# Performance work log

Measured on AMD Instinct MI355X. Metric: run time of the kernel, lower is better.

Reference implementation:

```python
import jax, jax.numpy as jnp
import numpy as np

B, S, D = 8, 2048, 256
EXP = 4
NEG = -1e9
EPS = 1e-5


def layer_norm(x, w, b):
    mu = jnp.mean(x, axis=-1, keepdims=True)
    var = jnp.var(x, axis=-1, keepdims=True)
    return (x - mu) * jax.lax.rsqrt(var + EPS) * w + b


def setup_inputs() -> dict:
    key = jax.random.key(0)
    ks = jax.random.split(key, 8)
    x = jax.random.normal(ks[0], (B, S, D), dtype=jnp.float32)
    r_mat = jax.random.normal(ks[1], (B, S, S), dtype=jnp.float32)
    attn_mask = jax.random.randint(ks[2], (S, S), 0, 2).astype(jnp.float32)
    pad_mask = jax.random.randint(ks[3], (B, 1, S), 0, 2).astype(jnp.float32)
    w1 = jax.random.normal(ks[4], (D, EXP * D), dtype=jnp.float32) / np.sqrt(D)
    b1 = jnp.zeros((EXP * D,), dtype=jnp.float32)
    w2 = jax.random.normal(ks[5], (EXP * D, D), dtype=jnp.float32) / np.sqrt(EXP * D)
    b2 = jnp.zeros((D,), dtype=jnp.float32)
    ln1_w = jnp.ones((D,), dtype=jnp.float32)
    ln1_b = jnp.zeros((D,), dtype=jnp.float32)
    ln2_w = jnp.ones((D,), dtype=jnp.float32)
    ln2_b = jnp.zeros((D,), dtype=jnp.float32)
    return {"x": x, "r_mat": r_mat, "attn_mask": attn_mask, "pad_mask": pad_mask,
            "ln1_w": ln1_w, "ln1_b": ln1_b, "ln2_w": ln2_w, "ln2_b": ln2_b,
            "w1": w1, "b1": b1, "w2": w2, "b2": b2}


def reference(x, r_mat, attn_mask, pad_mask, ln1_w, ln1_b, ln2_w, ln2_b, w1, b1, w2, b2):
    # sublayer 0: pre-LN + InrAwaSA + residual
    h = layer_norm(x, ln1_w, ln1_b)                       # [B,S,D]
    scale = jnp.sqrt(jnp.float32(D))
    scores = jnp.einsum("bqd,bkd->bqk", h, h) / scale      # [B,S,S]
    # mask r_mat by pad_mask [B,1,S] and attn_mask [1,S,S], then softmax
    rm = jnp.where(pad_mask == 0.0, NEG, r_mat)
    rm = jnp.where(attn_mask[None] == 0.0, NEG, rm)
    scores = scores + jax.nn.softmax(rm, axis=-1)
    # NOTE: the torch source calls scores.masked_fill(...) non-in-place and
    # discards the result, so scores are NOT re-masked here (faithful no-op).
    prob = jax.nn.softmax(scores, axis=-1)
    x = x + jnp.einsum("bqk,bkd->bqd", prob, h)
    # sublayer 1: pre-LN + FFN + residual (dropout is identity in eval)
    h2 = layer_norm(x, ln2_w, ln2_b)
    ffn = jax.nn.relu(h2 @ w1 + b1) @ w2 + b2
    return x + ffn
```

## Files before the change

kernel.cpp:

```cpp
#include <hip/hip_runtime.h>
#include <stdint.h>

#define NB 8
#define SS 2048
#define DD 256
#define NEGV -1e9f

typedef __attribute__((ext_vector_type(8))) __bf16 bf16x8;
typedef __attribute__((ext_vector_type(4))) float f32x4;

union U16 { uint4 u; bf16x8 b; unsigned short us[8]; };

__device__ __forceinline__ unsigned short tobf(float v) {
  union { float f; uint32_t u; } c; c.f = v;
  uint32_t r = (c.u + 0x7fffu + ((c.u >> 16) & 1u)) >> 16;
  return (unsigned short)r;
}
__device__ __forceinline__ float frombf(unsigned short v) {
  union { uint32_t u; float f; } c; c.u = ((uint32_t)v) << 16;
  return c.f;
}

__device__ __forceinline__ void glds16(const unsigned short* g, unsigned short* l) {
  __builtin_amdgcn_global_load_lds(
      (const __attribute__((address_space(1))) uint32_t*)g,
      (__attribute__((address_space(3))) uint32_t*)l, 16, 0, 0);
}

__device__ __forceinline__ void stage_tile(const unsigned short* src, int ld,
                                           unsigned short* lbuf, int w, int lane) {
  int rl = lane >> 2;
  int cs = (lane & 3) * 8;
  glds16(src + (size_t)(w * 32 + rl) * ld + cs, lbuf + w * 1024);
  glds16(src + (size_t)(w * 32 + 16 + rl) * ld + cs, lbuf + w * 1024 + 512);
}

template <int NSTEPS>
__device__ __forceinline__ void gemm128_tile(
    const unsigned short* __restrict__ A, int lda,
    const unsigned short* __restrict__ Bt, int ldb,
    unsigned short* lA, unsigned short* lB, f32x4 (&acc)[4][4]) {
  const int w = threadIdx.x >> 6, lane = threadIdx.x & 63;
  const int lr = lane & 15, lg = lane >> 4;
  const int wm = w >> 1, wn = w & 1;
#pragma unroll
  for (int i = 0; i < 4; ++i)
#pragma unroll
    for (int j = 0; j < 4; ++j) acc[i][j] = (f32x4){0.f, 0.f, 0.f, 0.f};
  stage_tile(A, lda, lA, w, lane);
  stage_tile(Bt, ldb, lB, w, lane);
  __syncthreads();
  for (int s = 0; s < NSTEPS; ++s) {
    const unsigned short* cA = lA + (s & 1) * 4096;
    const unsigned short* cB = lB + (s & 1) * 4096;
    if (s + 1 < NSTEPS) {
      stage_tile(A + (s + 1) * 32, lda, lA + ((s + 1) & 1) * 4096, w, lane);
      stage_tile(Bt + (s + 1) * 32, ldb, lB + ((s + 1) & 1) * 4096, w, lane);
    }
    bf16x8 am[4], bn[4];
#pragma unroll
    for (int i = 0; i < 4; ++i) {
      U16 u; u.u = *(const uint4*)(cA + (wm * 64 + i * 16 + lr) * 32 + lg * 8);
      am[i] = u.b;
      U16 v; v.u = *(const uint4*)(cB + (wn * 64 + i * 16 + lr) * 32 + lg * 8);
      bn[i] = v.b;
    }
#pragma unroll
    for (int i = 0; i < 4; ++i)
#pragma unroll
      for (int j = 0; j < 4; ++j)
        acc[i][j] = __builtin_amdgcn_mfma_f32_16x16x32_bf16(am[i], bn[j], acc[i][j], 0, 0, 0);
    __syncthreads();
  }
}

__global__ void ln_kernel(const float* __restrict__ in, const float* __restrict__ w,
                          const float* __restrict__ bparm, unsigned short* __restrict__ outb) {
  int row = blockIdx.x * 4 + (threadIdx.x >> 6);
  int lane = threadIdx.x & 63;
  const float* xr = in + (size_t)row * DD;
  float4 v = *(const float4*)(xr + lane * 4);
  float s = v.x + v.y + v.z + v.w;
  float s2 = v.x * v.x + v.y * v.y + v.z * v.z + v.w * v.w;
#pragma unroll
  for (int m = 1; m < 64; m <<= 1) { s += __shfl_xor(s, m); s2 += __shfl_xor(s2, m); }
  float mu = s * (1.f / DD);
  float var = s2 * (1.f / DD) - mu * mu;
  float rs = rsqrtf(var + 1e-5f);
  float4 wv = *(const float4*)(w + lane * 4);
  float4 bv = *(const float4*)(bparm + lane * 4);
  ushort4 o;
  o.x = tobf((v.x - mu) * rs * wv.x + bv.x);
  o.y = tobf((v.y - mu) * rs * wv.y + bv.y);
  o.z = tobf((v.z - mu) * rs * wv.z + bv.z);
  o.w = tobf((v.w - mu) * rs * wv.w + bv.w);
  *(ushort4*)(outb + (size_t)row * DD + lane * 4) = o;
}

__global__ void transpose_kernel(const unsigned short* __restrict__ in,
                                 unsigned short* __restrict__ out) {
  __shared__ unsigned short tile[64][72];
  int bid = blockIdx.x;
  int b = bid >> 7;
  int rest = bid & 127;
  int st = rest >> 2, dt = rest & 3;
  int s0 = st * 64, d0 = dt * 64;
  int t = threadIdx.x;
  int r = t >> 2, cs = (t & 3) * 16;
  const unsigned short* src = in + ((size_t)b * SS + s0 + r) * DD + d0 + cs;
  *(uint4*)&tile[r][cs] = *(const uint4*)src;
  *(uint4*)&tile[r][cs + 8] = *(const uint4*)(src + 8);
  __syncthreads();
  union { unsigned short us[16]; uint4 u[2]; } tmp;
  int dr = t >> 2, sseg = (t & 3) * 16;
#pragma unroll
  for (int j = 0; j < 16; ++j) tmp.us[j] = tile[sseg + j][dr];
  unsigned short* dst = out + ((size_t)b * DD + d0 + dr) * SS + s0 + sseg;
  *(uint4*)dst = tmp.u[0];
  *(uint4*)(dst + 8) = tmp.u[1];
}

__global__ __launch_bounds__(256) void qk_kernel(
    const unsigned short* __restrict__ hb,
    unsigned short* __restrict__ S) {
  __shared__ unsigned short lA[2 * 4096], lB[2 * 4096];
  int bid = blockIdx.x;
  int b = bid & 7;
  int tile = bid >> 3;
  int mb = tile >> 4, nb = tile & 15;
  const unsigned short* A = hb + (size_t)(b * SS + mb * 128) * DD;
  const unsigned short* Bt = hb + (size_t)(b * SS + nb * 128) * DD;
  f32x4 acc[4][4];
  gemm128_tile<8>(A, DD, Bt, DD, lA, lB, acc);
  int w = threadIdx.x >> 6, lane = threadIdx.x & 63;
  int lr = lane & 15, lg = lane >> 4;
  int wm = w >> 1, wn = w & 1;
  unsigned short* Sb = S + (size_t)b * SS * SS;
#pragma unroll
  for (int i = 0; i < 4; ++i)
#pragma unroll
    for (int j = 0; j < 4; ++j)
#pragma unroll
      for (int r = 0; r < 4; ++r) {
        int m = mb * 128 + wm * 64 + i * 16 + lg * 4 + r;
        int n = nb * 128 + wn * 64 + j * 16 + lr;
        Sb[(size_t)m * SS + n] = tobf(acc[i][j][r] * 0.0625f);
      }
}

__global__ __launch_bounds__(256) void smfuse_kernel(
    const float* __restrict__ r_mat,
    const float* __restrict__ attn,
    const float* __restrict__ pad,
    unsigned short* __restrict__ S) {
  int row = blockIdx.x * 4 + (threadIdx.x >> 6);
  int lane = threadIdx.x & 63;
  int b = row >> 11, q = row & 2047;
  const float* rrow = r_mat + (size_t)row * SS;
  const float* arow = attn + (size_t)q * SS;
  const float* prow = pad + (size_t)b * SS;
  unsigned short* srow = S + (size_t)row * SS;

  float rm[32];
  float mx = -__builtin_inff();
#pragma unroll
  for (int i = 0; i < 8; ++i) {
    int c = i * 256 + lane * 4;
    float4 rv = *(const float4*)(rrow + c);
    float4 av = *(const float4*)(arow + c);
    float4 pv = *(const float4*)(prow + c);
    float v0 = (pv.x == 0.f || av.x == 0.f) ? NEGV : rv.x;
    float v1 = (pv.y == 0.f || av.y == 0.f) ? NEGV : rv.y;
    float v2 = (pv.z == 0.f || av.z == 0.f) ? NEGV : rv.z;
    float v3 = (pv.w == 0.f || av.w == 0.f) ? NEGV : rv.w;
    rm[i * 4 + 0] = v0; rm[i * 4 + 1] = v1; rm[i * 4 + 2] = v2; rm[i * 4 + 3] = v3;
    mx = fmaxf(mx, fmaxf(fmaxf(v0, v1), fmaxf(v2, v3)));
  }
#pragma unroll
  for (int m = 1; m < 64; m <<= 1) mx = fmaxf(mx, __shfl_xor(mx, m));
  float sum = 0.f;
#pragma unroll
  for (int j = 0; j < 32; ++j) { rm[j] = __expf(rm[j] - mx); sum += rm[j]; }
#pragma unroll
  for (int m = 1; m < 64; m <<= 1) sum += __shfl_xor(sum, m);
  float inv = 1.f / sum;

  float sc[32];
  float mx2 = -__builtin_inff();
#pragma unroll
  for (int i = 0; i < 8; ++i) {
    int c = i * 256 + lane * 4;
    ushort4 sv = *(const ushort4*)(srow + c);
    float s0 = frombf(sv.x) + rm[i * 4 + 0] * inv;
    float s1 = frombf(sv.y) + rm[i * 4 + 1] * inv;
    float s2 = frombf(sv.z) + rm[i * 4 + 2] * inv;
    float s3 = frombf(sv.w) + rm[i * 4 + 3] * inv;
    sc[i * 4 + 0] = s0; sc[i * 4 + 1] = s1; sc[i * 4 + 2] = s2; sc[i * 4 + 3] = s3;
    mx2 = fmaxf(mx2, fmaxf(fmaxf(s0, s1), fmaxf(s2, s3)));
  }
#pragma unroll
  for (int m = 1; m < 64; m <<= 1) mx2 = fmaxf(mx2, __shfl_xor(mx2, m));
  float sum2 = 0.f;
#pragma unroll
  for (int j = 0; j < 32; ++j) { sc[j] = __expf(sc[j] - mx2); sum2 += sc[j]; }
#pragma unroll
  for (int m = 1; m < 64; m <<= 1) sum2 += __shfl_xor(sum2, m);
  float inv2 = 1.f / sum2;
#pragma unroll
  for (int i = 0; i < 8; ++i) {
    int c = i * 256 + lane * 4;
    ushort4 o;
    o.x = tobf(sc[i * 4 + 0] * inv2);
    o.y = tobf(sc[i * 4 + 1] * inv2);
    o.z = tobf(sc[i * 4 + 2] * inv2);
    o.w = tobf(sc[i * 4 + 3] * inv2);
    *(ushort4*)(srow + c) = o;
  }
}

__global__ __launch_bounds__(256) void pv_kernel(
    const unsigned short* __restrict__ P,
    const unsigned short* __restrict__ hbT,
    unsigned short* __restrict__ pvp) {
  __shared__ unsigned short lA[2 * 4096], lB[2 * 4096];
  int bid = blockIdx.x;
  int b = bid & 7;
  int rest = bid >> 3;
  int ks = rest & 3;
  int rest2 = rest >> 2;
  int nb = rest2 & 1, mb = rest2 >> 1;
  const unsigned short* A = P + (size_t)(b * SS + mb * 128) * SS + ks * 512;
  const unsigned short* Bt = hbT + (size_t)(b * DD + nb * 128) * SS + ks * 512;
  f32x4 acc[4][4];
  gemm128_tile<16>(A, SS, Bt, SS, lA, lB, acc);
  int w = threadIdx.x >> 6, lane = threadIdx.x & 63;
  int lr = lane & 15, lg = lane >> 4;
  int wm = w >> 1, wn = w & 1;
  unsigned short* O = pvp + ((size_t)(ks << 14) + (b << 11)) * DD;
#pragma unroll
  for (int i = 0; i < 4; ++i)
#pragma unroll
    for (int j = 0; j < 4; ++j)
#pragma unroll
      for (int r = 0; r < 4; ++r) {
        int m = mb * 128 + wm * 64 + i * 16 + lg * 4 + r;
        int n = nb * 128 + wn * 64 + j * 16 + lr;
        O[(size_t)m * DD + n] = tobf(acc[i][j][r]);
      }
}

__global__ __launch_bounds__(256) void pvreduce_kernel(
    const unsigned short* __restrict__ pvp,
    const float* __restrict__ x,
    const float* __restrict__ ln2w,
    const float* __restrict__ ln2b,
    float* __restrict__ out,
    unsigned short* __restrict__ h2b) {
  int r = blockIdx.x * 4 + (threadIdx.x >> 6);
  int lane = threadIdx.x & 63;
  int c = lane * 4;
  float o[4] = {0.f, 0.f, 0.f, 0.f};
#pragma unroll
  for (int ks = 0; ks < 4; ++ks) {
    ushort4 pk = *(const ushort4*)(pvp + ((size_t)(ks << 14) + r) * DD + c);
    o[0] += frombf(pk.x); o[1] += frombf(pk.y);
    o[2] += frombf(pk.z); o[3] += frombf(pk.w);
  }
  float4 xv = *(const float4*)(x + (size_t)r * DD + c);
  float val[4] = {o[0] + xv.x, o[1] + xv.y, o[2] + xv.z, o[3] + xv.w};
  float4 ov = {val[0], val[1], val[2], val[3]};
  *(float4*)(out + (size_t)r * DD + c) = ov;
  float s = val[0] + val[1] + val[2] + val[3];
  float s2 = val[0] * val[0] + val[1] * val[1] + val[2] * val[2] + val[3] * val[3];
#pragma unroll
  for (int m = 1; m < 64; m <<= 1) { s += __shfl_xor(s, m); s2 += __shfl_xor(s2, m); }
  float mu = s * (1.f / DD);
  float var = s2 * (1.f / DD) - mu * mu;
  float rsv = rsqrtf(var + 1e-5f);
  float4 wv = *(const float4*)(ln2w + c);
  float4 bv = *(const float4*)(ln2b + c);
  ushort4 h;
  h.x = tobf((val[0] - mu) * rsv * wv.x + bv.x);
  h.y = tobf((val[1] - mu) * rsv * wv.y + bv.y);
  h.z = tobf((val[2] - mu) * rsv * wv.z + bv.z);
  h.w = tobf((val[3] - mu) * rsv * wv.w + bv.w);
  *(ushort4*)(h2b + (size_t)r * DD + c) = h;
}

__global__ void wconv_kernel(const float* __restrict__ src, unsigned short* __restrict__ dst,
                             int K, int N) {
  int k = blockIdx.x;
  for (int n = threadIdx.x; n < N; n += 256)
    dst[(size_t)n * K + k] = tobf(src[(size_t)k * N + n]);
}

__global__ __launch_bounds__(256) void ffn1_kernel(
    const unsigned short* __restrict__ A0,
    const unsigned short* __restrict__ Bt0,
    const float* __restrict__ bias,
    unsigned short* __restrict__ Out) {
  __shared__ unsigned short lA[2 * 4096], lB[2 * 4096];
  int bid = blockIdx.x;
  int nb = bid & 7, mb = bid >> 3;
  const unsigned short* A = A0 + (size_t)(mb * 128) * 256;
  const unsigned short* Bt = Bt0 + (size_t)(nb * 128) * 256;
  f32x4 acc[4][4];
  gemm128_tile<8>(A, 256, Bt, 256, lA, lB, acc);
  int w = threadIdx.x >> 6, lane = threadIdx.x & 63;
  int lr = lane & 15, lg = lane >> 4;
  int wm = w >> 1, wn = w & 1;
#pragma unroll
  for (int i = 0; i < 4; ++i)
#pragma unroll
    for (int j = 0; j < 4; ++j)
#pragma unroll
      for (int r = 0; r < 4; ++r) {
        int m = mb * 128 + wm * 64 + i * 16 + lg * 4 + r;
        int n = nb * 128 + wn * 64 + j * 16 + lr;
        float v = fmaxf(acc[i][j][r] + bias[n], 0.f);
        Out[(size_t)m * 1024 + n] = tobf(v);
      }
}

__global__ __launch_bounds__(256) void ffn2_kernel(
    const unsigned short* __restrict__ A0,
    const unsigned short* __restrict__ Bt0,
    unsigned short* __restrict__ f2p) {
  __shared__ unsigned short lA[2 * 4096], lB[2 * 4096];
  int bid = blockIdx.x;
  int ks = bid & 3;
  int rest = bid >> 2;
  int nb = rest & 1, mb = rest >> 1;
  const unsigned short* A = A0 + (size_t)(mb * 128) * 1024 + ks * 256;
  const unsigned short* Bt = Bt0 + (size_t)(nb * 128) * 1024 + ks * 256;
  f32x4 acc[4][4];
  gemm128_tile<8>(A, 1024, Bt, 1024, lA, lB, acc);
  int w = threadIdx.x >> 6, lane = threadIdx.x & 63;
  int lr = lane & 15, lg = lane >> 4;
  int wm = w >> 1, wn = w & 1;
  unsigned short* O = f2p + (size_t)(ks << 14) * DD;
#pragma unroll
  for (int i = 0; i < 4; ++i)
#pragma unroll
    for (int j = 0; j < 4; ++j)
#pragma unroll
      for (int r = 0; r < 4; ++r) {
        int m = mb * 128 + wm * 64 + i * 16 + lg * 4 + r;
        int n = nb * 128 + wn * 64 + j * 16 + lr;
        O[(size_t)m * DD + n] = tobf(acc[i][j][r]);
      }
}

__global__ __launch_bounds__(256) void f2reduce_kernel(
    const unsigned short* __restrict__ f2p,
    const float* __restrict__ bias,
    float* __restrict__ out) {
  int r = blockIdx.x * 4 + (threadIdx.x >> 6);
  int lane = threadIdx.x & 63;
  int c = lane * 4;
  float o[4] = {0.f, 0.f, 0.f, 0.f};
#pragma unroll
  for (int ks = 0; ks < 4; ++ks) {
    ushort4 pk = *(const ushort4*)(f2p + ((size_t)(ks << 14) + r) * DD + c);
    o[0] += frombf(pk.x); o[1] += frombf(pk.y);
    o[2] += frombf(pk.z); o[3] += frombf(pk.w);
  }
  float4 bv = *(const float4*)(bias + c);
  float* orow = out + (size_t)r * DD + c;
  float4 cur = *(const float4*)orow;
  float4 res = {cur.x + o[0] + bv.x, cur.y + o[1] + bv.y,
                cur.z + o[2] + bv.z, cur.w + o[3] + bv.w};
  *(float4*)orow = res;
}

extern "C" void kernel_launch(void* const* d_in, const int* in_sizes, int n_in,
                              void* d_out, int out_size, void* d_ws, size_t ws_size,
                              hipStream_t stream) {
  const float* x     = (const float*)d_in[0];
  const float* r_mat = (const float*)d_in[1];
  const float* attn  = (const float*)d_in[2];
  const float* pad   = (const float*)d_in[3];
  const float* ln1w  = (const float*)d_in[4];
  const float* ln1b  = (const float*)d_in[5];
  const float* ln2w  = (const float*)d_in[6];
  const float* ln2b  = (const float*)d_in[7];
  const float* w1    = (const float*)d_in[8];
  const float* b1    = (const float*)d_in[9];
  const float* w2    = (const float*)d_in[10];
  const float* b2    = (const float*)d_in[11];
  float* out = (float*)d_out;

  uint8_t* ws = (uint8_t*)d_ws;
  unsigned short* hb   = (unsigned short*)(ws + 0);
  unsigned short* hbT  = (unsigned short*)(ws + 8388608);
  unsigned short* h2b  = (unsigned short*)(ws + 16777216);
  unsigned short* w1bT = (unsigned short*)(ws + 25165824);
  unsigned short* w2bT = (unsigned short*)(ws + 25690112);
  unsigned short* S    = (unsigned short*)(ws + 33554432);
  unsigned short* pvp  = (unsigned short*)(ws + 100663296);
  unsigned short* t    = S;
  unsigned short* f2p  = pvp;

  hipLaunchKernelGGL(ln_kernel, dim3(4096), dim3(256), 0, stream, x, ln1w, ln1b, hb);
  hipLaunchKernelGGL(transpose_kernel, dim3(1024), dim3(256), 0, stream, hb, hbT);
  hipLaunchKernelGGL(qk_kernel, dim3(2048), dim3(256), 0, stream, hb, S);
  hipLaunchKernelGGL(smfuse_kernel, dim3(4096), dim3(256), 0, stream, r_mat, attn, pad, S);
  hipLaunchKernelGGL(pv_kernel, dim3(1024), dim3(256), 0, stream, S, hbT, pvp);
  hipLaunchKernelGGL(pvreduce_kernel, dim3(4096), dim3(256), 0, stream,
                     pvp, x, ln2w, ln2b, out, h2b);
  hipLaunchKernelGGL(wconv_kernel, dim3(256), dim3(256), 0, stream, w1, w1bT, 256, 1024);
  hipLaunchKernelGGL(wconv_kernel, dim3(1024), dim3(256), 0, stream, w2, w2bT, 1024, 256);
  hipLaunchKernelGGL(ffn1_kernel, dim3(1024), dim3(256), 0, stream, h2b, w1bT, b1, t);
  hipLaunchKernelGGL(ffn2_kernel, dim3(1024), dim3(256), 0, stream, t, w2bT, f2p);
  hipLaunchKernelGGL(f2reduce_kernel, dim3(4096), dim3(256), 0, stream, f2p, b2, out);
}
```

Baseline: 201.5 us.

## Widen GEMM tiles to 128x256 with 512 threads and LDS-staged coalesced epilogue

Replaces the 128x128 GEMM tile with a 128x256 tile computed by 8 waves, which halves block counts and reuses each A tile across twice as many output columns. Epilogues now stage bf16 results through shared memory and write them with wide coalesced stores instead of scattered 2-byte stores. The weight-conversion kernel becomes a tiled LDS transpose with coalesced writes. The bigger tiles need more LDS per block, which may lower occupancy, and the epilogue adds extra barriers.

```diff
diff --git a/kernel.cpp b/kernel.cpp
--- a/kernel.cpp
+++ b/kernel.cpp
@@ -27,35 +27,36 @@
       (__attribute__((address_space(3))) uint32_t*)l, 16, 0, 0);
 }
 
-__device__ __forceinline__ void stage_tile(const unsigned short* src, int ld,
-                                           unsigned short* lbuf, int w, int lane) {
-  int rl = lane >> 2;
-  int cs = (lane & 3) * 8;
-  glds16(src + (size_t)(w * 32 + rl) * ld + cs, lbuf + w * 1024);
-  glds16(src + (size_t)(w * 32 + 16 + rl) * ld + cs, lbuf + w * 1024 + 512);
-}
-
 template <int NSTEPS>
-__device__ __forceinline__ void gemm128_tile(
+__device__ __forceinline__ void gemm256_acc(
     const unsigned short* __restrict__ A, int lda,
     const unsigned short* __restrict__ Bt, int ldb,
-    unsigned short* lA, unsigned short* lB, f32x4 (&acc)[4][4]) {
-  const int w = threadIdx.x >> 6, lane = threadIdx.x & 63;
+    unsigned short* smem, f32x4 (&acc)[4][4]) {
+  unsigned short* lA = smem;
+  unsigned short* lB = smem + 8192;
+  const int tid = threadIdx.x;
+  const int w = tid >> 6, lane = tid & 63;
   const int lr = lane & 15, lg = lane >> 4;
-  const int wm = w >> 1, wn = w & 1;
+  const int wm = w >> 2, wn = w & 3;
+  const int rl = lane >> 2, cs = (lane & 3) * 8;
 #pragma unroll
   for (int i = 0; i < 4; ++i)
 #pragma unroll
     for (int j = 0; j < 4; ++j) acc[i][j] = (f32x4){0.f, 0.f, 0.f, 0.f};
-  stage_tile(A, lda, lA, w, lane);
-  stage_tile(Bt, ldb, lB, w, lane);
+  glds16(A + (size_t)(w * 16 + rl) * lda + cs, lA + w * 512);
+  glds16(Bt + (size_t)(w * 32 + rl) * ldb + cs, lB + w * 1024);
+  glds16(Bt + (size_t)(w * 32 + 16 + rl) * ldb + cs, lB + w * 1024 + 512);
   __syncthreads();
   for (int s = 0; s < NSTEPS; ++s) {
     const unsigned short* cA = lA + (s & 1) * 4096;
-    const unsigned short* cB = lB + (s & 1) * 4096;
+    const unsigned short* cB = lB + (s & 1) * 8192;
     if (s + 1 < NSTEPS) {
-      stage_tile(A + (s + 1) * 32, lda, lA + ((s + 1) & 1) * 4096, w, lane);
-      stage_tile(Bt + (s + 1) * 32, ldb, lB + ((s + 1) & 1) * 4096, w, lane);
+      const unsigned short* An = A + (s + 1) * 32;
+      const unsigned short* Bn = Bt + (s + 1) * 32;
+      glds16(An + (size_t)(w * 16 + rl) * lda + cs, lA + ((s + 1) & 1) * 4096 + w * 512);
+      glds16(Bn + (size_t)(w * 32 + rl) * ldb + cs, lB + ((s + 1) & 1) * 8192 + w * 1024);
+      glds16(Bn + (size_t)(w * 32 + 16 + rl) * ldb + cs,
+             lB + ((s + 1) & 1) * 8192 + w * 1024 + 512);
     }
     bf16x8 am[4], bn[4];
 #pragma unroll
@@ -70,6 +71,46 @@
 #pragma unroll
       for (int j = 0; j < 4; ++j)
         acc[i][j] = __builtin_amdgcn_mfma_f32_16x16x32_bf16(am[i], bn[j], acc[i][j], 0, 0, 0);
+    __syncthreads();
+  }
+}
+
+template <int MODE>
+__device__ __forceinline__ void epi_store(
+    unsigned short* smem, f32x4 (&acc)[4][4],
+    unsigned short* dst, int ldd,
+    float scale, const float* bias, int n0) {
+  const int tid = threadIdx.x;
+  const int w = tid >> 6, lane = tid & 63;
+  const int lr = lane & 15, lg = lane >> 4;
+  const int wm = w >> 2, wn = w & 3;
+#pragma unroll
+  for (int c = 0; c < 2; ++c) {
+    if ((wn >> 1) == c) {
+#pragma unroll
+      for (int i = 0; i < 4; ++i)
+#pragma unroll
+        for (int j = 0; j < 4; ++j) {
+          int nl = (wn & 1) * 64 + j * 16 + lr;
+#pragma unroll
+          for (int r = 0; r < 4; ++r) {
+            int row = wm * 64 + i * 16 + lg * 4 + r;
+            float v = acc[i][j][r];
+            if (MODE == 0) v *= scale;
+            if (MODE == 2) v = fmaxf(v + bias[n0 + c * 128 + nl], 0.f);
+            smem[row * 128 + nl] = tobf(v);
+          }
+        }
+    }
+    __syncthreads();
+    int row = tid >> 2, cs2 = (tid & 3) * 32;
+    uint4 v0 = *(const uint4*)(smem + row * 128 + cs2);
+    uint4 v1 = *(const uint4*)(smem + row * 128 + cs2 + 8);
+    uint4 v2 = *(const uint4*)(smem + row * 128 + cs2 + 16);
+    uint4 v3 = *(const uint4*)(smem + row * 128 + cs2 + 24);
+    unsigned short* d = dst + (size_t)row * ldd + c * 128 + cs2;
+    *(uint4*)d = v0; *(uint4*)(d + 8) = v1;
+    *(uint4*)(d + 16) = v2; *(uint4*)(d + 24) = v3;
     __syncthreads();
   }
 }
@@ -120,32 +161,20 @@
   *(uint4*)(dst + 8) = tmp.u[1];
 }
 
-__global__ __launch_bounds__(256) void qk_kernel(
+__global__ __launch_bounds__(512) void qk_kernel(
     const unsigned short* __restrict__ hb,
     unsigned short* __restrict__ S) {
-  __shared__ unsigned short lA[2 * 4096], lB[2 * 4096];
+  __shared__ unsigned short smem[24576];
   int bid = blockIdx.x;
   int b = bid & 7;
-  int tile = bid >> 3;
-  int mb = tile >> 4, nb = tile & 15;
+  int t = bid >> 3;
+  int nb = t & 7, mb = t >> 3;
   const unsigned short* A = hb + (size_t)(b * SS + mb * 128) * DD;
-  const unsigned short* Bt = hb + (size_t)(b * SS + nb * 128) * DD;
+  const unsigned short* Bt = hb + (size_t)(b * SS + nb * 256) * DD;
   f32x4 acc[4][4];
-  gemm128_tile<8>(A, DD, Bt, DD, lA, lB, acc);
-  int w = threadIdx.x >> 6, lane = threadIdx.x & 63;
-  int lr = lane & 15, lg = lane >> 4;
-  int wm = w >> 1, wn = w & 1;
-  unsigned short* Sb = S + (size_t)b * SS * SS;
-#pragma unroll
-  for (int i = 0; i < 4; ++i)
-#pragma unroll
-    for (int j = 0; j < 4; ++j)
-#pragma unroll
-      for (int r = 0; r < 4; ++r) {
-        int m = mb * 128 + wm * 64 + i * 16 + lg * 4 + r;
-        int n = nb * 128 + wn * 64 + j * 16 + lr;
-        Sb[(size_t)m * SS + n] = tobf(acc[i][j][r] * 0.0625f);
-      }
+  gemm256_acc<8>(A, DD, Bt, DD, smem, acc);
+  unsigned short* dst = S + (size_t)b * SS * SS + (size_t)(mb * 128) * SS + nb * 256;
+  epi_store<0>(smem, acc, dst, SS, 0.0625f, nullptr, 0);
 }
 
 __global__ __launch_bounds__(256) void smfuse_kernel(
@@ -218,35 +247,21 @@
   }
 }
 
-__global__ __launch_bounds__(256) void pv_kernel(
+__global__ __launch_bounds__(512) void pv_kernel(
     const unsigned short* __restrict__ P,
     const unsigned short* __restrict__ hbT,
     unsigned short* __restrict__ pvp) {
-  __shared__ unsigned short lA[2 * 4096], lB[2 * 4096];
+  __shared__ unsigned short smem[24576];
   int bid = blockIdx.x;
   int b = bid & 7;
-  int rest = bid >> 3;
-  int ks = rest & 3;
-  int rest2 = rest >> 2;
-  int nb = rest2 & 1, mb = rest2 >> 1;
+  int r = bid >> 3;
+  int ks = r & 3, mb = r >> 2;
   const unsigned short* A = P + (size_t)(b * SS + mb * 128) * SS + ks * 512;
-  const unsigned short* Bt = hbT + (size_t)(b * DD + nb * 128) * SS + ks * 512;
+  const unsigned short* Bt = hbT + (size_t)(b * DD) * SS + ks * 512;
   f32x4 acc[4][4];
-  gemm128_tile<16>(A, SS, Bt, SS, lA, lB, acc);
-  int w = threadIdx.x >> 6, lane = threadIdx.x & 63;
-  int lr = lane & 15, lg = lane >> 4;
-  int wm = w >> 1, wn = w & 1;
-  unsigned short* O = pvp + ((size_t)(ks << 14) + (b << 11)) * DD;
-#pragma unroll
-  for (int i = 0; i < 4; ++i)
-#pragma unroll
-    for (int j = 0; j < 4; ++j)
-#pragma unroll
-      for (int r = 0; r < 4; ++r) {
-        int m = mb * 128 + wm * 64 + i * 16 + lg * 4 + r;
-        int n = nb * 128 + wn * 64 + j * 16 + lr;
-        O[(size_t)m * DD + n] = tobf(acc[i][j][r]);
-      }
+  gemm256_acc<16>(A, SS, Bt, SS, smem, acc);
+  unsigned short* dst = pvp + ((size_t)(ks << 14) + (b << 11) + mb * 128) * DD;
+  epi_store<1>(smem, acc, dst, DD, 1.f, nullptr, 0);
 }
 
 __global__ __launch_bounds__(256) void pvreduce_kernel(
@@ -289,66 +304,54 @@
 
 __global__ void wconv_kernel(const float* __restrict__ src, unsigned short* __restrict__ dst,
                              int K, int N) {
-  int k = blockIdx.x;
-  for (int n = threadIdx.x; n < N; n += 256)
-    dst[(size_t)n * K + k] = tobf(src[(size_t)k * N + n]);
-}
-
-__global__ __launch_bounds__(256) void ffn1_kernel(
+  __shared__ unsigned short tile[64][72];
+  int nt = N >> 6;
+  int kt = blockIdx.x / nt, ntb = blockIdx.x % nt;
+  int k0 = kt * 64, n0 = ntb * 64;
+  int t = threadIdx.x;
+  int r = t >> 2, c4 = (t & 3) * 16;
+  const float* s = src + (size_t)(k0 + r) * N + n0 + c4;
+#pragma unroll
+  for (int j = 0; j < 16; ++j) tile[r][c4 + j] = tobf(s[j]);
+  __syncthreads();
+  union { unsigned short us[16]; uint4 u[2]; } tmp;
+  int nr = t >> 2, ks = (t & 3) * 16;
+#pragma unroll
+  for (int j = 0; j < 16; ++j) tmp.us[j] = tile[ks + j][nr];
+  unsigned short* d = dst + (size_t)(n0 + nr) * K + k0 + ks;
+  *(uint4*)d = tmp.u[0];
+  *(uint4*)(d + 8) = tmp.u[1];
+}
+
+__global__ __launch_bounds__(512) void ffn1_kernel(
     const unsigned short* __restrict__ A0,
     const unsigned short* __restrict__ Bt0,
     const float* __restrict__ bias,
     unsigned short* __restrict__ Out) {
-  __shared__ unsigned short lA[2 * 4096], lB[2 * 4096];
+  __shared__ unsigned short smem[24576];
   int bid = blockIdx.x;
-  int nb = bid & 7, mb = bid >> 3;
+  int mb = bid & 127, nb = bid >> 7;
   const unsigned short* A = A0 + (size_t)(mb * 128) * 256;
-  const unsigned short* Bt = Bt0 + (size_t)(nb * 128) * 256;
+  const unsigned short* Bt = Bt0 + (size_t)(nb * 256) * 256;
   f32x4 acc[4][4];
-  gemm128_tile<8>(A, 256, Bt, 256, lA, lB, acc);
-  int w = threadIdx.x >> 6, lane = threadIdx.x & 63;
-  int lr = lane & 15, lg = lane >> 4;
-  int wm = w >> 1, wn = w & 1;
-#pragma unroll
-  for (int i = 0; i < 4; ++i)
-#pragma unroll
-    for (int j = 0; j < 4; ++j)
-#pragma unroll
-      for (int r = 0; r < 4; ++r) {
-        int m = mb * 128 + wm * 64 + i * 16 + lg * 4 + r;
-        int n = nb * 128 + wn * 64 + j * 16 + lr;
-        float v = fmaxf(acc[i][j][r] + bias[n], 0.f);
-        Out[(size_t)m * 1024 + n] = tobf(v);
-      }
-}
-
-__global__ __launch_bounds__(256) void ffn2_kernel(
+  gemm256_acc<8>(A, 256, Bt, 256, smem, acc);
+  unsigned short* dst = Out + (size_t)(mb * 128) * 1024 + nb * 256;
+  epi_store<2>(smem, acc, dst, 1024, 1.f, bias, nb * 256);
+}
+
+__global__ __launch_bounds__(512) void ffn2_kernel(
     const unsigned short* __restrict__ A0,
     const unsigned short* __restrict__ Bt0,
     unsigned short* __restrict__ f2p) {
-  __shared__ unsigned short lA[2 * 4096], lB[2 * 4096];
+  __shared__ unsigned short smem[24576];
   int bid = blockIdx.x;
-  int ks = bid & 3;
-  int rest = bid >> 2;
-  int nb = rest & 1, mb = rest >> 1;
+  int mb = bid & 127, ks = bid >> 7;
   const unsigned short* A = A0 + (size_t)(mb * 128) * 1024 + ks * 256;
-  const unsigned short* Bt = Bt0 + (size_t)(nb * 128) * 1024 + ks * 256;
+  const unsigned short* Bt = Bt0 + ks * 256;
   f32x4 acc[4][4];
-  gemm128_tile<8>(A, 1024, Bt, 1024, lA, lB, acc);
-  int w = threadIdx.x >> 6, lane = threadIdx.x & 63;
-  int lr = lane & 15, lg = lane >> 4;
-  int wm = w >> 1, wn = w & 1;
-  unsigned short* O = f2p + (size_t)(ks << 14) * DD;
-#pragma unroll
-  for (int i = 0; i < 4; ++i)
-#pragma unroll
-    for (int j = 0; j < 4; ++j)
-#pragma unroll
-      for (int r = 0; r < 4; ++r) {
-        int m = mb * 128 + wm * 64 + i * 16 + lg * 4 + r;
-        int n = nb * 128 + wn * 64 + j * 16 + lr;
-        O[(size_t)m * DD + n] = tobf(acc[i][j][r]);
-      }
+  gemm256_acc<8>(A, 1024, Bt, 1024, smem, acc);
+  unsigned short* dst = f2p + ((size_t)(ks << 14) + mb * 128) * DD;
+  epi_store<1>(smem, acc, dst, DD, 1.f, nullptr, 0);
 }
 
 __global__ __launch_bounds__(256) void f2reduce_kernel(
@@ -403,14 +406,14 @@
 
   hipLaunchKernelGGL(ln_kernel, dim3(4096), dim3(256), 0, stream, x, ln1w, ln1b, hb);
   hipLaunchKernelGGL(transpose_kernel, dim3(1024), dim3(256), 0, stream, hb, hbT);
-  hipLaunchKernelGGL(qk_kernel, dim3(2048), dim3(256), 0, stream, hb, S);
+  hipLaunchKernelGGL(qk_kernel, dim3(1024), dim3(512), 0, stream, hb, S);
   hipLaunchKernelGGL(smfuse_kernel, dim3(4096), dim3(256), 0, stream, r_mat, attn, pad, S);
-  hipLaunchKernelGGL(pv_kernel, dim3(1024), dim3(256), 0, stream, S, hbT, pvp);
+  hipLaunchKernelGGL(pv_kernel, dim3(512), dim3(512), 0, stream, S, hbT, pvp);
   hipLaunchKernelGGL(pvreduce_kernel, dim3(4096), dim3(256), 0, stream,
                      pvp, x, ln2w, ln2b, out, h2b);
-  hipLaunchKernelGGL(wconv_kernel, dim3(256), dim3(256), 0, stream, w1, w1bT, 256, 1024);
-  hipLaunchKernelGGL(wconv_kernel, dim3(1024), dim3(256), 0, stream, w2, w2bT, 1024, 256);
-  hipLaunchKernelGGL(ffn1_kernel, dim3(1024), dim3(256), 0, stream, h2b, w1bT, b1, t);
-  hipLaunchKernelGGL(ffn2_kernel, dim3(1024), dim3(256), 0, stream, t, w2bT, f2p);
+  hipLaunchKernelGGL(wconv_kernel, dim3(64), dim3(256), 0, stream, w1, w1bT, 256, 1024);
+  hipLaunchKernelGGL(wconv_kernel, dim3(64), dim3(256), 0, stream, w2, w2bT, 1024, 256);
+  hipLaunchKernelGGL(ffn1_kernel, dim3(512), dim3(512), 0, stream, h2b, w1bT, b1, t);
+  hipLaunchKernelGGL(ffn2_kernel, dim3(512), dim3(512), 0, stream, t, w2bT, f2p);
   hipLaunchKernelGGL(f2reduce_kernel, dim3(4096), dim3(256), 0, stream, f2p, b2, out);
 }
```

Result: slower. 227.0 us (+12.7%).

## Exploit symmetry of H·Hᵀ to compute only upper-triangle QK tiles; merge weight conversions

Applied to the files above, without the earlier changes.

The QK scores matrix is symmetric because both operands are the same normalized activations. The kernel now computes only the upper-triangular 128x128 tiles (136 per batch instead of 256) and writes each off-diagonal tile a second time, transposed through padded LDS, to the mirrored position. This roughly halves the MFMA work in the QK stage but adds an LDS transpose pass and a second full tile store. Separately, the two weight-conversion launches are merged into one kernel that uses an LDS-tiled transpose with coalesced accesses instead of strided scattered stores.

```diff
diff --git a/kernel.cpp b/kernel.cpp
--- a/kernel.cpp
+++ b/kernel.cpp
@@ -5,6 +5,7 @@
 #define SS 2048
 #define DD 256
 #define NEGV -1e9f
+#define LDSW 136
 
 typedef __attribute__((ext_vector_type(8))) __bf16 bf16x8;
 typedef __attribute__((ext_vector_type(4))) float f32x4;
@@ -39,7 +40,9 @@
 __device__ __forceinline__ void gemm128_tile(
     const unsigned short* __restrict__ A, int lda,
     const unsigned short* __restrict__ Bt, int ldb,
-    unsigned short* lA, unsigned short* lB, f32x4 (&acc)[4][4]) {
+    unsigned short* smem, f32x4 (&acc)[4][4]) {
+  unsigned short* lA = smem;
+  unsigned short* lB = smem + 8192;
   const int w = threadIdx.x >> 6, lane = threadIdx.x & 63;
   const int lr = lane & 15, lg = lane >> 4;
   const int wm = w >> 1, wn = w & 1;
@@ -123,16 +126,19 @@
 __global__ __launch_bounds__(256) void qk_kernel(
     const unsigned short* __restrict__ hb,
     unsigned short* __restrict__ S) {
-  __shared__ unsigned short lA[2 * 4096], lB[2 * 4096];
+  __shared__ unsigned short smem[17408];
   int bid = blockIdx.x;
   int b = bid & 7;
-  int tile = bid >> 3;
-  int mb = tile >> 4, nb = tile & 15;
+  int t = bid >> 3;
+  int mb = 0, rem = t;
+  while (rem >= 16 - mb) { rem -= 16 - mb; ++mb; }
+  int nb = mb + rem;
   const unsigned short* A = hb + (size_t)(b * SS + mb * 128) * DD;
   const unsigned short* Bt = hb + (size_t)(b * SS + nb * 128) * DD;
   f32x4 acc[4][4];
-  gemm128_tile<8>(A, DD, Bt, DD, lA, lB, acc);
-  int w = threadIdx.x >> 6, lane = threadIdx.x & 63;
+  gemm128_tile<8>(A, DD, Bt, DD, smem, acc);
+  int tid = threadIdx.x;
+  int w = tid >> 6, lane = tid & 63;
   int lr = lane & 15, lg = lane >> 4;
   int wm = w >> 1, wn = w & 1;
   unsigned short* Sb = S + (size_t)b * SS * SS;
@@ -146,6 +152,28 @@
         int n = nb * 128 + wn * 64 + j * 16 + lr;
         Sb[(size_t)m * SS + n] = tobf(acc[i][j][r] * 0.0625f);
       }
+  if (mb != nb) {
+#pragma unroll
+    for (int i = 0; i < 4; ++i)
+#pragma unroll
+      for (int j = 0; j < 4; ++j) {
+        int col = wn * 64 + j * 16 + lr;
+#pragma unroll
+        for (int r = 0; r < 4; ++r) {
+          int row = wm * 64 + i * 16 + lg * 4 + r;
+          smem[col * LDSW + row] = tobf(acc[i][j][r] * 0.0625f);
+        }
+      }
+    __syncthreads();
+    int row2 = tid >> 1, half = (tid & 1) * 64;
+    const unsigned short* s = smem + row2 * LDSW + half;
+    unsigned short* d = Sb + (size_t)(nb * 128 + row2) * SS + mb * 128 + half;
+    uint4 vv[8];
+#pragma unroll
+    for (int k = 0; k < 8; ++k) vv[k] = *(const uint4*)(s + k * 8);
+#pragma unroll
+    for (int k = 0; k < 8; ++k) *(uint4*)(d + k * 8) = vv[k];
+  }
 }
 
 __global__ __launch_bounds__(256) void smfuse_kernel(
@@ -222,7 +250,7 @@
     const unsigned short* __restrict__ P,
     const unsigned short* __restrict__ hbT,
     unsigned short* __restrict__ pvp) {
-  __shared__ unsigned short lA[2 * 4096], lB[2 * 4096];
+  __shared__ unsigned short smem[16384];
   int bid = blockIdx.x;
   int b = bid & 7;
   int rest = bid >> 3;
@@ -232,19 +260,19 @@
   const unsigned short* A = P + (size_t)(b * SS + mb * 128) * SS + ks * 512;
   const unsigned short* Bt = hbT + (size_t)(b * DD + nb * 128) * SS + ks * 512;
   f32x4 acc[4][4];
-  gemm128_tile<16>(A, SS, Bt, SS, lA, lB, acc);
+  gemm128_tile<16>(A, SS, Bt, SS, smem, acc);
   int w = threadIdx.x >> 6, lane = threadIdx.x & 63;
   int lr = lane & 15, lg = lane >> 4;
   int wm = w >> 1, wn = w & 1;
-  unsigned short* O = pvp + ((size_t)(ks << 14) + (b << 11)) * DD;
+  unsigned short* O = pvp + ((size_t)(ks << 14) + (b << 11) + mb * 128) * DD + nb * 128;
 #pragma unroll
   for (int i = 0; i < 4; ++i)
 #pragma unroll
     for (int j = 0; j < 4; ++j)
 #pragma unroll
       for (int r = 0; r < 4; ++r) {
-        int m = mb * 128 + wm * 64 + i * 16 + lg * 4 + r;
-        int n = nb * 128 + wn * 64 + j * 16 + lr;
+        int m = wm * 64 + i * 16 + lg * 4 + r;
+        int n = wn * 64 + j * 16 + lr;
         O[(size_t)m * DD + n] = tobf(acc[i][j][r]);
       }
 }
@@ -287,11 +315,29 @@
   *(ushort4*)(h2b + (size_t)r * DD + c) = h;
 }
 
-__global__ void wconv_kernel(const float* __restrict__ src, unsigned short* __restrict__ dst,
-                             int K, int N) {
-  int k = blockIdx.x;
-  for (int n = threadIdx.x; n < N; n += 256)
-    dst[(size_t)n * K + k] = tobf(src[(size_t)k * N + n]);
+__global__ void wconv_kernel(const float* __restrict__ w1, unsigned short* __restrict__ w1bT,
+                             const float* __restrict__ w2, unsigned short* __restrict__ w2bT) {
+  __shared__ unsigned short tile[64][72];
+  int bid = blockIdx.x;
+  const float* src; unsigned short* dst; int K, N, t;
+  if (bid < 64) { src = w1; dst = w1bT; K = 256; N = 1024; t = bid; }
+  else          { src = w2; dst = w2bT; K = 1024; N = 256; t = bid - 64; }
+  int nt = N >> 6;
+  int kt = t / nt, ntb = t % nt;
+  int k0 = kt * 64, n0 = ntb * 64;
+  int tt = threadIdx.x;
+  int r = tt >> 2, c4 = (tt & 3) * 16;
+  const float* s = src + (size_t)(k0 + r) * N + n0 + c4;
+#pragma unroll
+  for (int j = 0; j < 16; ++j) tile[r][c4 + j] = tobf(s[j]);
+  __syncthreads();
+  union { unsigned short us[16]; uint4 u[2]; } tmp;
+  int nr = tt >> 2, ks = (tt & 3) * 16;
+#pragma unroll
+  for (int j = 0; j < 16; ++j) tmp.us[j] = tile[ks + j][nr];
+  unsigned short* d = dst + (size_t)(n0 + nr) * K + k0 + ks;
+  *(uint4*)d = tmp.u[0];
+  *(uint4*)(d + 8) = tmp.u[1];
 }
 
 __global__ __launch_bounds__(256) void ffn1_kernel(
@@ -299,13 +345,13 @@
     const unsigned short* __restrict__ Bt0,
     const float* __restrict__ bias,
     unsigned short* __restrict__ Out) {
-  __shared__ unsigned short lA[2 * 4096], lB[2 * 4096];
+  __shared__ unsigned short smem[16384];
   int bid = blockIdx.x;
   int nb = bid & 7, mb = bid >> 3;
   const unsigned short* A = A0 + (size_t)(mb * 128) * 256;
   const unsigned short* Bt = Bt0 + (size_t)(nb * 128) * 256;
   f32x4 acc[4][4];
-  gemm128_tile<8>(A, 256, Bt, 256, lA, lB, acc);
+  gemm128_tile<8>(A, 256, Bt, 256, smem, acc);
   int w = threadIdx.x >> 6, lane = threadIdx.x & 63;
   int lr = lane & 15, lg = lane >> 4;
   int wm = w >> 1, wn = w & 1;
@@ -326,7 +372,7 @@
     const unsigned short* __restrict__ A0,
     const unsigned short* __restrict__ Bt0,
     unsigned short* __restrict__ f2p) {
-  __shared__ unsigned short lA[2 * 4096], lB[2 * 4096];
+  __shared__ unsigned short smem[16384];
   int bid = blockIdx.x;
   int ks = bid & 3;
   int rest = bid >> 2;
@@ -334,7 +380,7 @@
   const unsigned short* A = A0 + (size_t)(mb * 128) * 1024 + ks * 256;
   const unsigned short* Bt = Bt0 + (size_t)(nb * 128) * 1024 + ks * 256;
   f32x4 acc[4][4];
-  gemm128_tile<8>(A, 1024, Bt, 1024, lA, lB, acc);
+  gemm128_tile<8>(A, 1024, Bt, 1024, smem, acc);
   int w = threadIdx.x >> 6, lane = threadIdx.x & 63;
   int lr = lane & 15, lg = lane >> 4;
   int wm = w >> 1, wn = w & 1;
@@ -403,13 +449,12 @@
 
   hipLaunchKernelGGL(ln_kernel, dim3(4096), dim3(256), 0, stream, x, ln1w, ln1b, hb);
   hipLaunchKernelGGL(transpose_kernel, dim3(1024), dim3(256), 0, stream, hb, hbT);
-  hipLaunchKernelGGL(qk_kernel, dim3(2048), dim3(256), 0, stream, hb, S);
+  hipLaunchKernelGGL(qk_kernel, dim3(1088), dim3(256), 0, stream, hb, S);
   hipLaunchKernelGGL(smfuse_kernel, dim3(4096), dim3(256), 0, stream, r_mat, attn, pad, S);
   hipLaunchKernelGGL(pv_kernel, dim3(1024), dim3(256), 0, stream, S, hbT, pvp);
   hipLaunchKernelGGL(pvreduce_kernel, dim3(4096), dim3(256), 0, stream,
                      pvp, x, ln2w, ln2b, out, h2b);
-  hipLaunchKernelGGL(wconv_kernel, dim3(256), dim3(256), 0, stream, w1, w1bT, 256, 1024);
-  hipLaunchKernelGGL(wconv_kernel, dim3(1024), dim3(256), 0, stream, w2, w2bT, 1024, 256);
+  hipLaunchKernelGGL(wconv_kernel, dim3(128), dim3(256), 0, stream, w1, w1bT, w2, w2bT);
   hipLaunchKernelGGL(ffn1_kernel, dim3(1024), dim3(256), 0, stream, h2b, w1bT, b1, t);
   hipLaunchKernelGGL(ffn2_kernel, dim3(1024), dim3(256), 0, stream, t, w2bT, f2p);
   hipLaunchKernelGGL(f2reduce_kernel, dim3(4096), dim3(256), 0, stream, f2p, b2, out);
```

Measured after the change: 196.4 us. -2.5%, faster.
